# Optimization experiments

Measured on AMD Instinct MI355X. Metric: run time of the kernel, lower is better.

## Reference

```python
import jax, jax.numpy as jnp
import numpy as np
import math

NHEADS = 4


def _mab(Q, K, qw, qb, kw, kb, vw, vb, ow, ob, mask):
    """MAB2 from tripletformer: multi-head attention (head split via cat(split,0)),
    softmax scale uses sqrt(FULL dim_V), masked_fill(mask==0, -1e10), residual on
    the projected Q, then O + relu(fc_o(O))."""
    dv = qw.shape[1]
    dh = dv // NHEADS
    B, Nq, _ = Q.shape
    Nk = K.shape[1]
    Qh = (Q @ qw + qb).reshape(B, Nq, NHEADS, dh).transpose(0, 2, 1, 3)  # B,h,Nq,dh
    Kh = (K @ kw + kb).reshape(B, Nk, NHEADS, dh).transpose(0, 2, 1, 3)
    Vh = (K @ vw + vb).reshape(B, Nk, NHEADS, dh).transpose(0, 2, 1, 3)
    att = jnp.einsum('bhqd,bhkd->bhqk', Qh, Kh) * (1.0 / math.sqrt(dv))
    att = jnp.where(mask, att, jnp.asarray(-1e10, att.dtype))
    A = jax.nn.softmax(att, axis=-1)
    Oh = Qh + jnp.einsum('bhqk,bhkd->bhqd', A, Vh)
    O = Oh.transpose(0, 2, 1, 3).reshape(B, Nq, dv)
    return O + jax.nn.relu(O @ ow + ob)


def _forward(context_x, value, mask, obs_len, iff_w, iff_b, ind_points,
             q0w, q0b, k0w, k0b, v0w, v0b, o0w, o0b,
             q1w, q1b, k1w, k1b, v1w, v1b, o1w, o1b):
    B, L = context_x.shape
    D = value.shape[-1]
    mflat = mask.reshape(B, L * D)
    # stable stream compaction: observed entries first, original (time-major,
    # channel-minor) order preserved; truncate to static obs_len
    order = jnp.argsort(-mflat, axis=-1, stable=True)[:, :obs_len]  # (B, N)
    T = jnp.broadcast_to(context_x[:, :, None], (B, L, D)).reshape(B, L * D)
    C = jnp.broadcast_to(jnp.arange(D, dtype=jnp.int32), (B, L, D)).reshape(B, L * D)
    U = value.reshape(B, L * D)
    take = lambda a: jnp.take_along_axis(a, order, axis=-1)
    T_, U_, mk_ = take(T), take(U), take(mflat)
    Ch = jax.nn.one_hot(take(C), D, dtype=value.dtype)  # one_hot(num_classes=dim-2)
    X = jnp.concatenate([Ch, T_[..., None], U_[..., None]], axis=-1) * mk_[..., None]
    Y = jax.nn.relu(X @ iff_w + iff_b) * mk_[..., None]
    key_valid = mk_ > 0                        # (B, N)
    mask1 = key_valid[:, None, None, :]        # mab0: mask padded keys
    mask2 = key_valid[:, None, :, None]        # mab1: mask padded query rows
    Z = Y
    n_layers = ind_points.shape[0]
    for i in range(n_layers):
        I = jnp.broadcast_to(ind_points[i], (B,) + ind_points[i].shape)
        H = _mab(I, Z, q0w[i], q0b[i], k0w[i], k0b[i], v0w[i], v0b[i], o0w[i], o0b[i], mask1)
        Zn = _mab(Z, H, q1w[i], q1b[i], k1w[i], k1b[i], v1w[i], v1b[i], o1w[i], o1b[i], mask2)
        Z = Zn * mk_[..., None] + Z
    return Z, mk_[..., None]


def setup_inputs() -> dict:
    B, L, D, OBS, DK, M, NL = 16, 512, 41, 4096, 128, 128, 3
    key = jax.random.key(0)
    ks = jax.random.split(key, 16)
    context_x = jnp.sort(jax.random.uniform(ks[0], (B, L), dtype=jnp.float32), axis=-1)
    value = jax.random.normal(ks[1], (B, L, D), dtype=jnp.float32)
    # exactly OBS observed entries per batch row -> static packed length
    r = jax.random.uniform(ks[2], (B, L * D))
    kth = jnp.sort(r, axis=-1)[:, OBS]
    mask = (r < kth[:, None]).astype(jnp.float32).reshape(B, L, D)

    def w(k, shape, fan):
        return jax.random.normal(k, shape, dtype=jnp.float32) / math.sqrt(fan)

    inp = dict(
        context_x=context_x, value=value, mask=mask, obs_len=OBS,
        iff_w=w(ks[3], (D + 2, DK), D + 2), iff_b=jnp.zeros((DK,), jnp.float32),
        ind_points=w(ks[4], (NL, M, DK), DK),
    )
    for j, n in enumerate(['q0', 'k0', 'v0', 'o0', 'q1', 'k1', 'v1', 'o1']):
        inp[n + 'w'] = w(ks[5 + j], (NL, DK, DK), DK)
        inp[n + 'b'] = jnp.zeros((NL, DK), jnp.float32)
    return inp


def reference(context_x, value, mask, obs_len, iff_w, iff_b, ind_points,
              q0w, q0b, k0w, k0b, v0w, v0b, o0w, o0b,
              q1w, q1b, k1w, k1b, v1w, v1b, o1w, o1b):
    return _forward(context_x, value, mask, obs_len, iff_w, iff_b, ind_points,
                    q0w, q0b, k0w, k0b, v0w, v0b, o0w, o0b,
                    q1w, q1b, k1w, k1b, v1w, v1b, o1w, o1b)
```

## Files before the change

kernel.cpp:

```cpp
#include <hip/hip_runtime.h>
#include <math.h>

#define NBATCH 16
#define SEQL   512
#define DIM    41
#define LDFLAT (SEQL*DIM)
#define OBS    4096
#define DK     128
#define NH     4
#define DH     32

typedef short bf16x8 __attribute__((ext_vector_type(8)));
typedef short short8v __attribute__((ext_vector_type(8)));
typedef float floatx4 __attribute__((ext_vector_type(4)));

__device__ __forceinline__ short f2bf(float f) {
  union { float f; unsigned u; } v;
  v.f = f;
  unsigned r = (v.u + 0x7fffu + ((v.u >> 16) & 1u)) >> 16;
  return (short)r;
}
__device__ __forceinline__ float bf2f(short s) {
  union { unsigned u; float f; } v;
  v.u = ((unsigned)(unsigned short)s) << 16;
  return v.f;
}

__device__ __forceinline__ void stage_w(short* Wl, const short* __restrict__ Wt,
                                        int tid) {
#pragma unroll
  for (int i = tid * 8; i < 128 * 128; i += 2048)
    *(int4*)&Wl[(i >> 7) * 136 + (i & 127)] = *(const int4*)&Wt[i];
}
__device__ __forceinline__ void load_af(const short* Xl, int wv, int lm,
                                        int quad, bf16x8 af[4]) {
#pragma unroll
  for (int kc = 0; kc < 4; kc++)
    af[kc] = *(bf16x8*)&Xl[(wv * 16 + lm) * 136 + kc * 32 + quad * 8];
}
__device__ __forceinline__ void gemm8(const short* Wl, const bf16x8 af[4],
                                      int lm, int quad, floatx4 acc[8]) {
#pragma unroll
  for (int nt = 0; nt < 8; nt++) acc[nt] = (floatx4){0.f, 0.f, 0.f, 0.f};
#pragma unroll
  for (int kc = 0; kc < 4; kc++) {
    bf16x8 a = af[kc];
#pragma unroll
    for (int nt = 0; nt < 8; nt++) {
      bf16x8 b = *(bf16x8*)&Wl[(nt * 16 + lm) * 136 + kc * 32 + quad * 8];
      acc[nt] = __builtin_amdgcn_mfma_f32_16x16x32_bf16(a, b, acc[nt], 0, 0, 0);
    }
  }
}
__device__ __forceinline__ void store_sl(short* Sl, const floatx4 acc[8],
                                         const float* __restrict__ bias,
                                         int wv, int lm, int quad) {
#pragma unroll
  for (int nt = 0; nt < 8; nt++) {
    int col = nt * 16 + lm;
    float bn = bias[col];
#pragma unroll
    for (int r = 0; r < 4; r++)
      Sl[(wv * 16 + quad * 4 + r) * 136 + col] = f2bf(acc[nt][r] + bn);
  }
}
__device__ __forceinline__ void write_hs(const short* Sl,
                                         short* __restrict__ out, int rb,
                                         int nshift, int tid) {
  int rr = tid >> 2, hh = tid & 3;
  int r = rb + rr;
  int bb = r >> nshift, nn = r & ((1 << nshift) - 1);
  size_t o = (((size_t)(bb * NH + hh) << nshift) + nn) * 32;
#pragma unroll
  for (int j = 0; j < 4; j++)
    *(int4*)&out[o + j * 8] = *(int4*)&Sl[rr * 136 + hh * 32 + j * 8];
}

__global__ __launch_bounds__(256) void prep_weights_kernel(
    const float* __restrict__ q0w, const float* __restrict__ k0w,
    const float* __restrict__ v0w, const float* __restrict__ o0w,
    const float* __restrict__ q1w, const float* __restrict__ k1w,
    const float* __restrict__ v1w, const float* __restrict__ o1w,
    short* __restrict__ Wt) {
  __shared__ float Tl[128 * 132];
  int id = blockIdx.x, l = id >> 3, wi = id & 7;
  const float* s;
  switch (wi) {
    case 0: s = q0w; break; case 1: s = k0w; break;
    case 2: s = v0w; break; case 3: s = o0w; break;
    case 4: s = q1w; break; case 5: s = k1w; break;
    case 6: s = v1w; break; default: s = o1w; break;
  }
  s += (size_t)l * 16384;
  int tid = threadIdx.x;
  for (int i = tid * 4; i < 16384; i += 1024) {
    int k = i >> 7, n = i & 127;
    float4 x = *(const float4*)&s[i];
    Tl[k * 132 + n + 0] = x.x; Tl[k * 132 + n + 1] = x.y;
    Tl[k * 132 + n + 2] = x.z; Tl[k * 132 + n + 3] = x.w;
  }
  __syncthreads();
  short* dst = Wt + (size_t)id * 16384;
  int n = tid >> 1, k0 = (tid & 1) * 64;
  for (int jc = 0; jc < 8; jc++) {
    short8v t;
#pragma unroll
    for (int j = 0; j < 8; j++) t[j] = f2bf(Tl[(k0 + jc * 8 + j) * 132 + n]);
    *(short8v*)&dst[n * 128 + k0 + jc * 8] = t;
  }
}

__global__ __launch_bounds__(1024) void build_order_kernel(
    const float* __restrict__ mask, int* __restrict__ order,
    float* __restrict__ mk_out, float* __restrict__ mk_out2) {
  int b = blockIdx.x;
  const float* m = mask + (size_t)b * LDFLAT;
  int tid = threadIdx.x;
  int lane = tid & 63, w = tid >> 6;
  __shared__ int wsums[16];
  __shared__ int s_total_ones;
  __shared__ int s_chunk_ones;
  __shared__ int s_ones_base;
  __shared__ int s_zeros_base;

  int cnt = 0;
  for (int j = tid; j < LDFLAT; j += 1024) cnt += (m[j] > 0.f) ? 1 : 0;
  for (int off = 32; off > 0; off >>= 1) cnt += __shfl_xor(cnt, off);
  if (lane == 0) wsums[w] = cnt;
  __syncthreads();
  if (tid == 0) {
    int t = 0;
    for (int i = 0; i < 16; i++) t += wsums[i];
    s_total_ones = t; s_ones_base = 0; s_zeros_base = 0;
  }
  __syncthreads();
  int total_ones = s_total_ones;

  for (int c0 = 0; c0 < LDFLAT; c0 += 1024) {
    __syncthreads();
    int j = c0 + tid;
    bool valid = (j < LDFLAT);
    float mv = valid ? m[j] : 0.f;
    int one = (valid && mv > 0.f) ? 1 : 0;
    int v = one;
    for (int off = 1; off < 64; off <<= 1) {
      int t = __shfl_up(v, (unsigned)off);
      if (lane >= off) v += t;
    }
    if (lane == 63) wsums[w] = v;
    __syncthreads();
    if (tid == 0) {
      int run = 0;
      for (int i = 0; i < 16; i++) { int t = wsums[i]; wsums[i] = run; run += t; }
      s_chunk_ones = run;
    }
    __syncthreads();
    int ones_before = (v - one) + wsums[w];
    int ob = s_ones_base, zb = s_zeros_base, chunk_ones = s_chunk_ones;
    int rem = LDFLAT - c0;
    int chunk_valid = rem < 1024 ? rem : 1024;
    int valid_before = tid < rem ? tid : rem;
    if (valid) {
      int pos = one ? (ob + ones_before)
                    : (total_ones + zb + (valid_before - ones_before));
      if (pos < OBS) {
        order[b * OBS + pos] = j;
        mk_out[b * OBS + pos] = mv;
        mk_out2[b * OBS + pos] = mv;
      }
    }
    __syncthreads();
    if (tid == 0) {
      s_ones_base = ob + chunk_ones;
      s_zeros_base = zb + (chunk_valid - chunk_ones);
    }
  }
}

__global__ __launch_bounds__(256) void qh_proj_kernel(
    const float* __restrict__ indp, const short* __restrict__ Wt,
    const float* __restrict__ q0b, short* __restrict__ qh_b) {
  __shared__ __align__(16) short Xl[64 * 136];
  __shared__ __align__(16) short Wl[128 * 136];
  int l = blockIdx.y, rb = blockIdx.x * 64;
  const float* X = indp + (size_t)l * 16384 + (size_t)rb * 128;
  const short* W = Wt + (size_t)(l * 8) * 16384;
  const float* bias = q0b + (size_t)l * 128;
  short* out = qh_b + (size_t)l * 16384;
  int tid = threadIdx.x;
  for (int i = tid * 4; i < 64 * 128; i += 1024) {
    int rr = i >> 7, c = i & 127;
    float4 x = *(const float4*)&X[i];
    *(short4*)&Xl[rr * 136 + c] =
        make_short4(f2bf(x.x), f2bf(x.y), f2bf(x.z), f2bf(x.w));
  }
  stage_w(Wl, W, tid);
  __syncthreads();
  int wv = tid >> 6, lane = tid & 63, lm = lane & 15, quad = lane >> 4;
  bf16x8 af[4];
  load_af(Xl, wv, lm, quad, af);
  floatx4 acc[8];
  gemm8(Wl, af, lm, quad, acc);
  __syncthreads();
  store_sl(Wl, acc, bias, wv, lm, quad);
  __syncthreads();
  write_hs(Wl, out, rb, 7, tid);
}

__global__ __launch_bounds__(256) void fusedA_kernel(
    const int* __restrict__ order, const float* __restrict__ mk_g,
    const float* __restrict__ cx, const float* __restrict__ value,
    const float* __restrict__ iff_w, const float* __restrict__ iff_b,
    float* __restrict__ Z,
    const short* __restrict__ Wk, const float* __restrict__ kbias,
    short* __restrict__ Kb,
    const short* __restrict__ Wv, const float* __restrict__ vbias,
    short* __restrict__ Vb,
    const short* __restrict__ Wq, const float* __restrict__ qbias,
    short* __restrict__ Qb) {
  __shared__ __align__(16) short Xl[64 * 136];
  __shared__ __align__(16) short Wl[128 * 136];
  __shared__ int   rdd[64];
  __shared__ float rdt[64], rdu[64], rdm[64];
  int tid = threadIdx.x;
  int rb = blockIdx.x * 64;
  if (tid < 64) {
    int idx = rb + tid;
    int b = idx >> 12;
    int j = order[idx];
    int l = j / DIM;
    rdd[tid] = j - l * DIM;
    rdt[tid] = cx[b * SEQL + l];
    rdu[tid] = value[(size_t)b * LDFLAT + j];
    rdm[tid] = mk_g[idx];
  }
  stage_w(Wl, Wk, tid);
  __syncthreads();
  for (int i = tid; i < 64 * 128; i += 256) {
    int rr = i >> 7, k = i & 127;
    float y = iff_w[rdd[rr] * DK + k] + rdt[rr] * iff_w[41 * DK + k] +
              rdu[rr] * iff_w[42 * DK + k] + iff_b[k];
    float z = fmaxf(y, 0.f) * rdm[rr];
    Z[(size_t)(rb + rr) * DK + k] = z;
    Xl[rr * 136 + k] = f2bf(z);
  }
  __syncthreads();
  int wv = tid >> 6, lane = tid & 63, lm = lane & 15, quad = lane >> 4;
  bf16x8 af[4];
  load_af(Xl, wv, lm, quad, af);
  floatx4 acc[8];
  gemm8(Wl, af, lm, quad, acc);
  __syncthreads();
  store_sl(Wl, acc, kbias, wv, lm, quad);
  __syncthreads();
  write_hs(Wl, Kb, rb, 12, tid);
  __syncthreads();
  stage_w(Wl, Wv, tid);
  __syncthreads();
  gemm8(Wl, af, lm, quad, acc);
  __syncthreads();
  store_sl(Wl, acc, vbias, wv, lm, quad);
  __syncthreads();
  write_hs(Wl, Vb, rb, 12, tid);
  __syncthreads();
  stage_w(Wl, Wq, tid);
  __syncthreads();
  gemm8(Wl, af, lm, quad, acc);
  __syncthreads();
  store_sl(Wl, acc, qbias, wv, lm, quad);
  __syncthreads();
  write_hs(Wl, Qb, rb, 12, tid);
}

__global__ __launch_bounds__(256) void attn1_kernel(
    const short* __restrict__ Qh,
    const short* __restrict__ Kh, const short* __restrict__ Vh,
    const float* __restrict__ mk,
    float* __restrict__ Opart, float* __restrict__ mpart,
    float* __restrict__ lpart) {
  __shared__ __align__(16) short Ql[128 * 40];
  __shared__ __align__(16) short Kc[64 * 40];
  __shared__ __align__(16) short Vtc[32 * 72];
  __shared__ __align__(16) short Pl[128 * 72];
  __shared__ float mkc[64];
  int bh = blockIdx.x;
  int b = bh >> 2, h = bh & 3;
  int ks = blockIdx.y;
  int tid = threadIdx.x;
  int wv = tid >> 6, lane = tid & 63, lm = lane & 15, quad = lane >> 4;

  const short* qbg = Qh + (size_t)h * 128 * 32;
  for (int i = tid * 8; i < 128 * 32; i += 2048) {
    int r = i >> 5, c = i & 31;
    *(int4*)&Ql[r * 40 + c] = *(const int4*)&qbg[i];
  }
  __syncthreads();
  bf16x8 aq[2];
  aq[0] = *(bf16x8*)&Ql[(wv * 32 + lm) * 40 + quad * 8];
  aq[1] = *(bf16x8*)&Ql[(wv * 32 + 16 + lm) * 40 + quad * 8];

  float m_i[2][4], l_i[2][4];
  floatx4 oacc[2][2];
#pragma unroll
  for (int mt = 0; mt < 2; mt++) {
#pragma unroll
    for (int r = 0; r < 4; r++) { m_i[mt][r] = -1e30f; l_i[mt][r] = 0.f; }
    oacc[mt][0] = (floatx4){0.f, 0.f, 0.f, 0.f};
    oacc[mt][1] = (floatx4){0.f, 0.f, 0.f, 0.f};
  }
  const float scale = 0.08838834764831845f;
  const short* kbase = Kh + ((size_t)bh * OBS + ks * 512) * 32;
  const short* vbase = Vh + ((size_t)bh * OBS + ks * 512) * 32;
  const float* mkb = mk + (size_t)b * OBS + ks * 512;

  for (int ch = 0; ch < 8; ch++) {
    __syncthreads();
    {
      int i = tid * 8;
      int r = i >> 5, c = i & 31;
      *(int4*)&Kc[r * 40 + c] = *(const int4*)&kbase[ch * 2048 + i];
      int4 vv4 = *(const int4*)&vbase[ch * 2048 + i];
      short* vv = (short*)&vv4;
#pragma unroll
      for (int j = 0; j < 8; j++) Vtc[(c + j) * 72 + r] = vv[j];
    }
    if (tid < 64) mkc[tid] = mkb[ch * 64 + tid];
    __syncthreads();

    floatx4 sf[2][4];
#pragma unroll
    for (int nt = 0; nt < 4; nt++) {
      bf16x8 bfrag = *(bf16x8*)&Kc[(nt * 16 + lm) * 40 + quad * 8];
      floatx4 z = {0.f, 0.f, 0.f, 0.f};
      sf[0][nt] = __builtin_amdgcn_mfma_f32_16x16x32_bf16(aq[0], bfrag, z, 0, 0, 0);
      sf[1][nt] = __builtin_amdgcn_mfma_f32_16x16x32_bf16(aq[1], bfrag, z, 0, 0, 0);
    }
#pragma unroll
    for (int nt = 0; nt < 4; nt++) {
      float mkv = mkc[nt * 16 + lm];
      bool ok = mkv > 0.f;
#pragma unroll
      for (int mt = 0; mt < 2; mt++)
#pragma unroll
        for (int r = 0; r < 4; r++)
          sf[mt][nt][r] = ok ? sf[mt][nt][r] * scale : -1e10f;
    }
#pragma unroll
    for (int mt = 0; mt < 2; mt++) {
#pragma unroll
      for (int r = 0; r < 4; r++) {
        float mx = fmaxf(fmaxf(sf[mt][0][r], sf[mt][1][r]),
                         fmaxf(sf[mt][2][r], sf[mt][3][r]));
        mx = fmaxf(mx, __shfl_xor(mx, 1));
        mx = fmaxf(mx, __shfl_xor(mx, 2));
        mx = fmaxf(mx, __shfl_xor(mx, 4));
        mx = fmaxf(mx, __shfl_xor(mx, 8));
        float mn = fmaxf(m_i[mt][r], mx);
        float al = __expf(m_i[mt][r] - mn);
        float ps = 0.f;
#pragma unroll
        for (int nt = 0; nt < 4; nt++) {
          float p = __expf(sf[mt][nt][r] - mn);
          sf[mt][nt][r] = p;
          ps += p;
        }
        ps += __shfl_xor(ps, 1);
        ps += __shfl_xor(ps, 2);
        ps += __shfl_xor(ps, 4);
        ps += __shfl_xor(ps, 8);
        l_i[mt][r] = l_i[mt][r] * al + ps;
        m_i[mt][r] = mn;
        oacc[mt][0] *= al;
        oacc[mt][1] *= al;
      }
    }
#pragma unroll
    for (int mt = 0; mt < 2; mt++)
#pragma unroll
      for (int nt = 0; nt < 4; nt++)
#pragma unroll
        for (int r = 0; r < 4; r++)
          Pl[(wv * 32 + mt * 16 + quad * 4 + r) * 72 + nt * 16 + lm] =
              f2bf(sf[mt][nt][r]);
#pragma unroll
    for (int kc = 0; kc < 2; kc++) {
      bf16x8 vf0 = *(bf16x8*)&Vtc[lm * 72 + kc * 32 + quad * 8];
      bf16x8 vf1 = *(bf16x8*)&Vtc[(16 + lm) * 72 + kc * 32 + quad * 8];
#pragma unroll
      for (int mt = 0; mt < 2; mt++) {
        bf16x8 pf = *(bf16x8*)&Pl[(wv * 32 + mt * 16 + lm) * 72 + kc * 32 + quad * 8];
        oacc[mt][0] = __builtin_amdgcn_mfma_f32_16x16x32_bf16(pf, vf0, oacc[mt][0], 0, 0, 0);
        oacc[mt][1] = __builtin_amdgcn_mfma_f32_16x16x32_bf16(pf, vf1, oacc[mt][1], 0, 0, 0);
      }
    }
  }
  float* ob = Opart + (size_t)(ks * 64 + bh) * 128 * 32;
#pragma unroll
  for (int mt = 0; mt < 2; mt++) {
#pragma unroll
    for (int r = 0; r < 4; r++) {
      int row = wv * 32 + mt * 16 + quad * 4 + r;
      ob[(size_t)row * 32 + lm] = oacc[mt][0][r];
      ob[(size_t)row * 32 + 16 + lm] = oacc[mt][1][r];
      if (lm == 0) {
        mpart[(size_t)(ks * 64 + bh) * 128 + row] = m_i[mt][r];
        lpart[(size_t)(ks * 64 + bh) * 128 + row] = l_i[mt][r];
      }
    }
  }
}

__global__ __launch_bounds__(256) void fusedB_kernel(
    const float* __restrict__ Opart, const float* __restrict__ mpart,
    const float* __restrict__ lpart, const short* __restrict__ qh,
    const short* __restrict__ Wo, const float* __restrict__ obias,
    const short* __restrict__ Wk, const float* __restrict__ kbias,
    const short* __restrict__ Wv, const float* __restrict__ vbias,
    short* __restrict__ khb, short* __restrict__ vhb) {
  __shared__ __align__(16) short Xl[64 * 136];
  __shared__ __align__(16) short Wl[128 * 136];
  int tid = threadIdx.x;
  int rb = blockIdx.x * 64;
  int b = rb >> 7, n0 = rb & 127;
  {
    int rr = tid >> 2, hh = tid & 3;
    int n = n0 + rr;
    int bh = b * 4 + hh;
    float mv[8], lv[8], m = -1e30f;
#pragma unroll
    for (int s = 0; s < 8; s++) {
      mv[s] = mpart[(size_t)(s * 64 + bh) * 128 + n];
      lv[s] = lpart[(size_t)(s * 64 + bh) * 128 + n];
      m = fmaxf(m, mv[s]);
    }
    float l = 0.f;
    float oa[32];
#pragma unroll
    for (int d = 0; d < 32; d++) oa[d] = 0.f;
#pragma unroll
    for (int s = 0; s < 8; s++) {
      float w = __expf(mv[s] - m);
      l += lv[s] * w;
      const float* op = &Opart[((size_t)(s * 64 + bh) * 128 + n) * 32];
#pragma unroll
      for (int d4 = 0; d4 < 8; d4++) {
        float4 v = *(const float4*)&op[d4 * 4];
        oa[d4 * 4 + 0] += v.x * w; oa[d4 * 4 + 1] += v.y * w;
        oa[d4 * 4 + 2] += v.z * w; oa[d4 * 4 + 3] += v.w * w;
      }
    }
    float li = 1.f / l;
    const short* qp = &qh[((size_t)hh * 128 + n) * 32];
#pragma unroll
    for (int d = 0; d < 32; d++)
      Xl[rr * 136 + hh * 32 + d] = f2bf(bf2f(qp[d]) + oa[d] * li);
  }
  stage_w(Wl, Wo, tid);
  __syncthreads();
  int wv = tid >> 6, lane = tid & 63, lm = lane & 15, quad = lane >> 4;
  bf16x8 af[4];
  load_af(Xl, wv, lm, quad, af);
  floatx4 acc[8];
  gemm8(Wl, af, lm, quad, acc);
  __syncthreads();
#pragma unroll
  for (int nt = 0; nt < 8; nt++) {
    int col = nt * 16 + lm;
    float bn = obias[col];
#pragma unroll
    for (int r = 0; r < 4; r++) {
      int row = wv * 16 + quad * 4 + r;
      float ov = bf2f(Xl[row * 136 + col]);
      Wl[row * 136 + col] = f2bf(ov + fmaxf(acc[nt][r] + bn, 0.f));
    }
  }
  __syncthreads();
  for (int i = tid * 8; i < 64 * 128; i += 2048)
    *(int4*)&Xl[(i >> 7) * 136 + (i & 127)] = *(int4*)&Wl[(i >> 7) * 136 + (i & 127)];
  __syncthreads();
  load_af(Xl, wv, lm, quad, af);
  stage_w(Wl, Wk, tid);
  __syncthreads();
  gemm8(Wl, af, lm, quad, acc);
  __syncthreads();
  store_sl(Wl, acc, kbias, wv, lm, quad);
  __syncthreads();
  write_hs(Wl, khb, rb, 7, tid);
  __syncthreads();
  stage_w(Wl, Wv, tid);
  __syncthreads();
  gemm8(Wl, af, lm, quad, acc);
  __syncthreads();
  store_sl(Wl, acc, vbias, wv, lm, quad);
  __syncthreads();
  write_hs(Wl, vhb, rb, 7, tid);
}

__global__ __launch_bounds__(256) void attn2_kernel(
    const short* __restrict__ Qh, const short* __restrict__ Kh,
    const short* __restrict__ Vh, short* __restrict__ O) {
  __shared__ __align__(16) short Kl[128 * 40];
  __shared__ __align__(16) short Vt[32 * 136];
  __shared__ __align__(16) short Ql[64 * 40];
  __shared__ __align__(16) short Pl[64 * 136];
  int bh = blockIdx.x;
  int b = bh >> 2, h = bh & 3;
  int q0 = blockIdx.y * 64;
  int tid = threadIdx.x;
  int wv = tid >> 6, lane = tid & 63, lm = lane & 15, quad = lane >> 4;
  const short* kb = Kh + (size_t)bh * 128 * 32;
  const short* vb = Vh + (size_t)bh * 128 * 32;
  const short* qb = Qh + ((size_t)bh * OBS + q0) * 32;

  for (int i = tid * 8; i < 128 * 32; i += 2048) {
    int r = i >> 5, c = i & 31;
    *(int4*)&Kl[r * 40 + c] = *(const int4*)&kb[i];
  }
  for (int i = tid * 8; i < 64 * 32; i += 2048) {
    int r = i >> 5, c = i & 31;
    *(int4*)&Ql[r * 40 + c] = *(const int4*)&qb[i];
  }
  for (int i = tid * 8; i < 128 * 32; i += 2048) {
    int r = i >> 5, c = i & 31;
    int4 vv4 = *(const int4*)&vb[i];
    short* vv = (short*)&vv4;
#pragma unroll
    for (int j = 0; j < 8; j++) Vt[(c + j) * 136 + r] = vv[j];
  }
  __syncthreads();

  const float scale = 0.08838834764831845f;
  bf16x8 afrag = *(bf16x8*)&Ql[(wv * 16 + lm) * 40 + quad * 8];
  floatx4 sf[8];
#pragma unroll
  for (int nt = 0; nt < 8; nt++) {
    bf16x8 bfrag = *(bf16x8*)&Kl[(nt * 16 + lm) * 40 + quad * 8];
    floatx4 z = {0.f, 0.f, 0.f, 0.f};
    sf[nt] = __builtin_amdgcn_mfma_f32_16x16x32_bf16(afrag, bfrag, z, 0, 0, 0);
  }
#pragma unroll
  for (int nt = 0; nt < 8; nt++) sf[nt] *= scale;
  float linv[4];
#pragma unroll
  for (int r = 0; r < 4; r++) {
    float mx = sf[0][r];
#pragma unroll
    for (int nt = 1; nt < 8; nt++) mx = fmaxf(mx, sf[nt][r]);
    mx = fmaxf(mx, __shfl_xor(mx, 1));
    mx = fmaxf(mx, __shfl_xor(mx, 2));
    mx = fmaxf(mx, __shfl_xor(mx, 4));
    mx = fmaxf(mx, __shfl_xor(mx, 8));
    float sum = 0.f;
#pragma unroll
    for (int nt = 0; nt < 8; nt++) {
      float p = __expf(sf[nt][r] - mx);
      sf[nt][r] = p;
      sum += p;
    }
    sum += __shfl_xor(sum, 1);
    sum += __shfl_xor(sum, 2);
    sum += __shfl_xor(sum, 4);
    sum += __shfl_xor(sum, 8);
    linv[r] = 1.f / sum;
  }
#pragma unroll
  for (int nt = 0; nt < 8; nt++)
#pragma unroll
    for (int r = 0; r < 4; r++)
      Pl[(wv * 16 + quad * 4 + r) * 136 + nt * 16 + lm] = f2bf(sf[nt][r]);
  __syncthreads();

  floatx4 oacc[2] = {{0.f, 0.f, 0.f, 0.f}, {0.f, 0.f, 0.f, 0.f}};
#pragma unroll
  for (int kc = 0; kc < 4; kc++) {
    bf16x8 pf = *(bf16x8*)&Pl[(wv * 16 + lm) * 136 + kc * 32 + quad * 8];
#pragma unroll
    for (int nt2 = 0; nt2 < 2; nt2++) {
      bf16x8 vf = *(bf16x8*)&Vt[(nt2 * 16 + lm) * 136 + kc * 32 + quad * 8];
      oacc[nt2] = __builtin_amdgcn_mfma_f32_16x16x32_bf16(pf, vf, oacc[nt2], 0, 0, 0);
    }
  }
  __syncthreads();
  short* Ol = Pl;
#pragma unroll
  for (int nt2 = 0; nt2 < 2; nt2++) {
#pragma unroll
    for (int r = 0; r < 4; r++) {
      int qrow = wv * 16 + quad * 4 + r;
      float q = bf2f(Ql[qrow * 40 + nt2 * 16 + lm]);
      Ol[qrow * 136 + nt2 * 16 + lm] = f2bf(q + oacc[nt2][r] * linv[r]);
    }
  }
  __syncthreads();
  int rr = tid >> 2, seg = tid & 3;
  size_t o = ((size_t)b * OBS + q0 + rr) * 128 + h * 32 + seg * 8;
  *(int4*)&O[o] = *(int4*)&Ol[rr * 136 + seg * 8];
}

__global__ __launch_bounds__(256) void fusedC_kernel(
    const short* __restrict__ Ob, const short* __restrict__ Wo,
    const float* __restrict__ obias, const float* __restrict__ mk,
    const float* __restrict__ Zin, float* __restrict__ Zout,
    const short* __restrict__ Wk, const float* __restrict__ kbias,
    short* __restrict__ Kb,
    const short* __restrict__ Wv, const float* __restrict__ vbias,
    short* __restrict__ Vb,
    const short* __restrict__ Wq, const float* __restrict__ qbias,
    short* __restrict__ Qb) {
  __shared__ __align__(16) short Xl[64 * 136];
  __shared__ __align__(16) short Wl[128 * 136];
  int tid = threadIdx.x;
  int rb = blockIdx.x * 64;
  for (int i = tid * 8; i < 64 * 128; i += 2048) {
    int rr = i >> 7, c = i & 127;
    *(int4*)&Xl[rr * 136 + c] = *(const int4*)&Ob[(size_t)(rb + rr) * 128 + c];
  }
  stage_w(Wl, Wo, tid);
  __syncthreads();
  int wv = tid >> 6, lane = tid & 63, lm = lane & 15, quad = lane >> 4;
  bf16x8 af[4];
  load_af(Xl, wv, lm, quad, af);
  floatx4 acc[8];
  gemm8(Wl, af, lm, quad, acc);
  __syncthreads();
  float* Fl = (float*)Wl;
#pragma unroll
  for (int nt = 0; nt < 8; nt++) {
    int col = nt * 16 + lm;
    float bn = obias[col];
#pragma unroll
    for (int r = 0; r < 4; r++) {
      int row = wv * 16 + quad * 4 + r;
      int gr = rb + row;
      float ov = bf2f(Xl[row * 136 + col]);
      float f = ov + fmaxf(acc[nt][r] + bn, 0.f);
      Fl[row * 132 + col] = Zin[(size_t)gr * 128 + col] + f * mk[gr];
    }
  }
  __syncthreads();
  {
    int rr = tid >> 2, seg = tid & 3;
    int gr = rb + rr;
#pragma unroll
    for (int j = 0; j < 8; j++) {
      float4 f = *(float4*)&Fl[rr * 132 + seg * 32 + j * 4];
      *(float4*)&Zout[(size_t)gr * 128 + seg * 32 + j * 4] = f;
      *(short4*)&Xl[rr * 136 + seg * 32 + j * 4] =
          make_short4(f2bf(f.x), f2bf(f.y), f2bf(f.z), f2bf(f.w));
    }
  }
  if (Wk == nullptr) return;
  __syncthreads();
  load_af(Xl, wv, lm, quad, af);
  stage_w(Wl, Wk, tid);
  __syncthreads();
  gemm8(Wl, af, lm, quad, acc);
  __syncthreads();
  store_sl(Wl, acc, kbias, wv, lm, quad);
  __syncthreads();
  write_hs(Wl, Kb, rb, 12, tid);
  __syncthreads();
  stage_w(Wl, Wv, tid);
  __syncthreads();
  gemm8(Wl, af, lm, quad, acc);
  __syncthreads();
  store_sl(Wl, acc, vbias, wv, lm, quad);
  __syncthreads();
  write_hs(Wl, Vb, rb, 12, tid);
  __syncthreads();
  stage_w(Wl, Wq, tid);
  __syncthreads();
  gemm8(Wl, af, lm, quad, acc);
  __syncthreads();
  store_sl(Wl, acc, qbias, wv, lm, quad);
  __syncthreads();
  write_hs(Wl, Qb, rb, 12, tid);
}

extern "C" void kernel_launch(void* const* d_in, const int* in_sizes, int n_in,
                              void* d_out, int out_size, void* d_ws,
                              size_t ws_size, hipStream_t stream) {
  const float* cx    = (const float*)d_in[0];
  const float* value = (const float*)d_in[1];
  const float* mask  = (const float*)d_in[2];
  const float* iff_w = (const float*)d_in[4];
  const float* iff_b = (const float*)d_in[5];
  const float* indp  = (const float*)d_in[6];
  const float* q0w = (const float*)d_in[7];  const float* q0b = (const float*)d_in[8];
  const float* k0w = (const float*)d_in[9];  const float* k0b = (const float*)d_in[10];
  const float* v0w = (const float*)d_in[11]; const float* v0b = (const float*)d_in[12];
  const float* o0w = (const float*)d_in[13]; const float* o0b = (const float*)d_in[14];
  const float* q1w = (const float*)d_in[15]; const float* q1b = (const float*)d_in[16];
  const float* k1w = (const float*)d_in[17]; const float* k1b = (const float*)d_in[18];
  const float* v1w = (const float*)d_in[19]; const float* v1b = (const float*)d_in[20];
  const float* o1w = (const float*)d_in[21]; const float* o1b = (const float*)d_in[22];

  char* ws = (char*)d_ws;
  short* Wt    = (short*)ws;  ws += (size_t)24 * 16384 * 2;
  int*   order = (int*)ws;    ws += (size_t)NBATCH * OBS * 4;
  float* mk_g  = (float*)ws;  ws += (size_t)NBATCH * OBS * 4;
  float* Z     = (float*)ws;  ws += (size_t)NBATCH * OBS * DK * 4;
  short* Qb    = (short*)ws;  ws += (size_t)NBATCH * OBS * DK * 2;
  short* Kb    = (short*)ws;  ws += (size_t)NBATCH * OBS * DK * 2;
  short* Vb    = (short*)ws;  ws += (size_t)NBATCH * OBS * DK * 2;
  short* Ob    = (short*)ws;  ws += (size_t)NBATCH * OBS * DK * 2;
  short* qh_b  = (short*)ws;  ws += (size_t)3 * 128 * DK * 2;
  short* khb   = (short*)ws;  ws += (size_t)NBATCH * NH * 128 * DH * 2;
  short* vhb   = (short*)ws;  ws += (size_t)NBATCH * NH * 128 * DH * 2;
  float* Opart = (float*)ws;  ws += (size_t)8 * 64 * 128 * 32 * 4;
  float* mpart = (float*)ws;  ws += (size_t)8 * 64 * 128 * 4;
  float* lpart = (float*)ws;  ws += (size_t)8 * 64 * 128 * 4;

  float* outZ  = (float*)d_out;
  float* outMk = outZ + (size_t)NBATCH * OBS * DK;

  prep_weights_kernel<<<24, 256, 0, stream>>>(q0w, k0w, v0w, o0w, q1w, k1w,
                                              v1w, o1w, Wt);
  build_order_kernel<<<NBATCH, 1024, 0, stream>>>(mask, order, mk_g, outMk);
  qh_proj_kernel<<<dim3(2, 3), 256, 0, stream>>>(indp, Wt, q0b, qh_b);

  const short* W[3][8];
  for (int l = 0; l < 3; l++)
    for (int wi = 0; wi < 8; wi++) W[l][wi] = Wt + (size_t)(l * 8 + wi) * 16384;

  fusedA_kernel<<<1024, 256, 0, stream>>>(
      order, mk_g, cx, value, iff_w, iff_b, Z,
      W[0][1], k0b, Kb, W[0][2], v0b, Vb, W[0][4], q1b, Qb);

  for (int l = 0; l < 3; l++) {
    attn1_kernel<<<dim3(64, 8), 256, 0, stream>>>(
        qh_b + (size_t)l * 16384, Kb, Vb, mk_g, Opart, mpart, lpart);
    fusedB_kernel<<<32, 256, 0, stream>>>(
        Opart, mpart, lpart, qh_b + (size_t)l * 16384,
        W[l][3], o0b + (size_t)l * 128,
        W[l][5], k1b + (size_t)l * 128,
        W[l][6], v1b + (size_t)l * 128, khb, vhb);
    attn2_kernel<<<dim3(64, 64), 256, 0, stream>>>(Qb, khb, vhb, Ob);
    if (l < 2) {
      fusedC_kernel<<<1024, 256, 0, stream>>>(
          Ob, W[l][7], o1b + (size_t)l * 128, mk_g, Z, Z,
          W[l + 1][1], k0b + (size_t)(l + 1) * 128, Kb,
          W[l + 1][2], v0b + (size_t)(l + 1) * 128, Vb,
          W[l + 1][4], q1b + (size_t)(l + 1) * 128, Qb);
    } else {
      fusedC_kernel<<<1024, 256, 0, stream>>>(
          Ob, W[l][7], o1b + (size_t)l * 128, mk_g, Z, outZ,
          nullptr, nullptr, nullptr, nullptr, nullptr, nullptr,
          nullptr, nullptr, nullptr);
    }
  }
}
```

Measured before the change: 530.8 us.

## Prefetch next weight tile into registers and store GEMM outputs directly to global

Weight matrices for the next projection (V, Q, K) are loaded into registers while the current MFMA GEMM runs, then committed to shared memory, which overlaps global loads with compute. The LDS staging round-trip for outputs is removed: results are written straight to head-split global layout from the accumulators. fusedC reads its input A-fragments and residuals directly from global memory. The cost is more register pressure and narrower (2-byte, scattered) global stores in place of coalesced 16-byte writes.

New measurement: 572.2 us. +7.8%, slower.

```diff
diff --git a/kernel.cpp b/kernel.cpp
--- a/kernel.cpp
+++ b/kernel.cpp
@@ -32,11 +32,33 @@
   for (int i = tid * 8; i < 128 * 128; i += 2048)
     *(int4*)&Wl[(i >> 7) * 136 + (i & 127)] = *(const int4*)&Wt[i];
 }
+__device__ __forceinline__ void prefetch_w(const short* __restrict__ Wt,
+                                           int tid, int4 wreg[8]) {
+#pragma unroll
+  for (int j = 0; j < 8; j++)
+    wreg[j] = *(const int4*)&Wt[tid * 8 + j * 2048];
+}
+__device__ __forceinline__ void commit_w(short* Wl, int tid,
+                                         const int4 wreg[8]) {
+#pragma unroll
+  for (int j = 0; j < 8; j++) {
+    int i = tid * 8 + j * 2048;
+    *(int4*)&Wl[(i >> 7) * 136 + (i & 127)] = wreg[j];
+  }
+}
 __device__ __forceinline__ void load_af(const short* Xl, int wv, int lm,
                                         int quad, bf16x8 af[4]) {
 #pragma unroll
   for (int kc = 0; kc < 4; kc++)
     af[kc] = *(bf16x8*)&Xl[(wv * 16 + lm) * 136 + kc * 32 + quad * 8];
+}
+__device__ __forceinline__ void load_af_global(const short* __restrict__ X,
+                                               int row0, int wv, int lm,
+                                               int quad, bf16x8 af[4]) {
+  const short* rp = X + (size_t)(row0 + wv * 16 + lm) * 128;
+#pragma unroll
+  for (int kc = 0; kc < 4; kc++)
+    af[kc] = *(const bf16x8*)&rp[kc * 32 + quad * 8];
 }
 __device__ __forceinline__ void gemm8(const short* Wl, const bf16x8 af[4],
                                       int lm, int quad, floatx4 acc[8]) {
@@ -52,28 +74,25 @@
     }
   }
 }
-__device__ __forceinline__ void store_sl(short* Sl, const floatx4 acc[8],
+__device__ __forceinline__ void store_hs(short* __restrict__ out,
+                                         const floatx4 acc[8],
                                          const float* __restrict__ bias,
-                                         int wv, int lm, int quad) {
+                                         int rb, int nshift, int wv, int lm,
+                                         int quad) {
 #pragma unroll
   for (int nt = 0; nt < 8; nt++) {
     int col = nt * 16 + lm;
     float bn = bias[col];
-#pragma unroll
-    for (int r = 0; r < 4; r++)
-      Sl[(wv * 16 + quad * 4 + r) * 136 + col] = f2bf(acc[nt][r] + bn);
-  }
-}
-__device__ __forceinline__ void write_hs(const short* Sl,
-                                         short* __restrict__ out, int rb,
-                                         int nshift, int tid) {
-  int rr = tid >> 2, hh = tid & 3;
-  int r = rb + rr;
-  int bb = r >> nshift, nn = r & ((1 << nshift) - 1);
-  size_t o = (((size_t)(bb * NH + hh) << nshift) + nn) * 32;
-#pragma unroll
-  for (int j = 0; j < 4; j++)
-    *(int4*)&out[o + j * 8] = *(int4*)&Sl[rr * 136 + hh * 32 + j * 8];
+    int hh = nt >> 1;
+    int dd = (nt & 1) * 16 + lm;
+#pragma unroll
+    for (int r = 0; r < 4; r++) {
+      int gr = rb + wv * 16 + quad * 4 + r;
+      int bb = gr >> nshift, nn = gr & ((1 << nshift) - 1);
+      out[(((size_t)(bb * NH + hh) << nshift) + nn) * 32 + dd] =
+          f2bf(acc[nt][r] + bn);
+    }
+  }
 }
 
 __global__ __launch_bounds__(256) void prep_weights_kernel(
@@ -201,10 +220,7 @@
   load_af(Xl, wv, lm, quad, af);
   floatx4 acc[8];
   gemm8(Wl, af, lm, quad, acc);
-  __syncthreads();
-  store_sl(Wl, acc, bias, wv, lm, quad);
-  __syncthreads();
-  write_hs(Wl, out, rb, 7, tid);
+  store_hs(out, acc, bias, rb, 7, wv, lm, quad);
 }
 
 __global__ __launch_bounds__(256) void fusedA_kernel(
@@ -248,28 +264,22 @@
   int wv = tid >> 6, lane = tid & 63, lm = lane & 15, quad = lane >> 4;
   bf16x8 af[4];
   load_af(Xl, wv, lm, quad, af);
+  int4 wreg[8];
+  prefetch_w(Wv, tid, wreg);
   floatx4 acc[8];
   gemm8(Wl, af, lm, quad, acc);
-  __syncthreads();
-  store_sl(Wl, acc, kbias, wv, lm, quad);
-  __syncthreads();
-  write_hs(Wl, Kb, rb, 12, tid);
-  __syncthreads();
-  stage_w(Wl, Wv, tid);
-  __syncthreads();
-  gemm8(Wl, af, lm, quad, acc);
-  __syncthreads();
-  store_sl(Wl, acc, vbias, wv, lm, quad);
-  __syncthreads();
-  write_hs(Wl, Vb, rb, 12, tid);
-  __syncthreads();
-  stage_w(Wl, Wq, tid);
-  __syncthreads();
-  gemm8(Wl, af, lm, quad, acc);
-  __syncthreads();
-  store_sl(Wl, acc, qbias, wv, lm, quad);
-  __syncthreads();
-  write_hs(Wl, Qb, rb, 12, tid);
+  store_hs(Kb, acc, kbias, rb, 12, wv, lm, quad);
+  __syncthreads();
+  commit_w(Wl, tid, wreg);
+  prefetch_w(Wq, tid, wreg);
+  __syncthreads();
+  gemm8(Wl, af, lm, quad, acc);
+  store_hs(Vb, acc, vbias, rb, 12, wv, lm, quad);
+  __syncthreads();
+  commit_w(Wl, tid, wreg);
+  __syncthreads();
+  gemm8(Wl, af, lm, quad, acc);
+  store_hs(Qb, acc, qbias, rb, 12, wv, lm, quad);
 }
 
 __global__ __launch_bounds__(256) void attn1_kernel(
@@ -456,13 +466,14 @@
       Xl[rr * 136 + hh * 32 + d] = f2bf(bf2f(qp[d]) + oa[d] * li);
   }
   stage_w(Wl, Wo, tid);
+  int4 wreg[8];
+  prefetch_w(Wk, tid, wreg);
   __syncthreads();
   int wv = tid >> 6, lane = tid & 63, lm = lane & 15, quad = lane >> 4;
   bf16x8 af[4];
   load_af(Xl, wv, lm, quad, af);
   floatx4 acc[8];
   gemm8(Wl, af, lm, quad, acc);
-  __syncthreads();
 #pragma unroll
   for (int nt = 0; nt < 8; nt++) {
     int col = nt * 16 + lm;
@@ -471,29 +482,21 @@
     for (int r = 0; r < 4; r++) {
       int row = wv * 16 + quad * 4 + r;
       float ov = bf2f(Xl[row * 136 + col]);
-      Wl[row * 136 + col] = f2bf(ov + fmaxf(acc[nt][r] + bn, 0.f));
-    }
-  }
-  __syncthreads();
-  for (int i = tid * 8; i < 64 * 128; i += 2048)
-    *(int4*)&Xl[(i >> 7) * 136 + (i & 127)] = *(int4*)&Wl[(i >> 7) * 136 + (i & 127)];
-  __syncthreads();
+      Xl[row * 136 + col] = f2bf(ov + fmaxf(acc[nt][r] + bn, 0.f));
+    }
+  }
+  __syncthreads();
+  commit_w(Wl, tid, wreg);
+  prefetch_w(Wv, tid, wreg);
   load_af(Xl, wv, lm, quad, af);
-  stage_w(Wl, Wk, tid);
-  __syncthreads();
-  gemm8(Wl, af, lm, quad, acc);
-  __syncthreads();
-  store_sl(Wl, acc, kbias, wv, lm, quad);
-  __syncthreads();
-  write_hs(Wl, khb, rb, 7, tid);
-  __syncthreads();
-  stage_w(Wl, Wv, tid);
-  __syncthreads();
-  gemm8(Wl, af, lm, quad, acc);
-  __syncthreads();
-  store_sl(Wl, acc, vbias, wv, lm, quad);
-  __syncthreads();
-  write_hs(Wl, vhb, rb, 7, tid);
+  __syncthreads();
+  gemm8(Wl, af, lm, quad, acc);
+  store_hs(khb, acc, kbias, rb, 7, wv, lm, quad);
+  __syncthreads();
+  commit_w(Wl, tid, wreg);
+  __syncthreads();
+  gemm8(Wl, af, lm, quad, acc);
+  store_hs(vhb, acc, vbias, rb, 7, wv, lm, quad);
 }
 
 __global__ __launch_bounds__(256) void attn2_kernel(
@@ -580,21 +583,16 @@
       oacc[nt2] = __builtin_amdgcn_mfma_f32_16x16x32_bf16(pf, vf, oacc[nt2], 0, 0, 0);
     }
   }
-  __syncthreads();
-  short* Ol = Pl;
 #pragma unroll
   for (int nt2 = 0; nt2 < 2; nt2++) {
 #pragma unroll
     for (int r = 0; r < 4; r++) {
       int qrow = wv * 16 + quad * 4 + r;
       float q = bf2f(Ql[qrow * 40 + nt2 * 16 + lm]);
-      Ol[qrow * 136 + nt2 * 16 + lm] = f2bf(q + oacc[nt2][r] * linv[r]);
-    }
-  }
-  __syncthreads();
-  int rr = tid >> 2, seg = tid & 3;
-  size_t o = ((size_t)b * OBS + q0 + rr) * 128 + h * 32 + seg * 8;
-  *(int4*)&O[o] = *(int4*)&Ol[rr * 136 + seg * 8];
+      O[((size_t)b * OBS + q0 + qrow) * 128 + h * 32 + nt2 * 16 + lm] =
+          f2bf(q + oacc[nt2][r] * linv[r]);
+    }
+  }
 }
 
 __global__ __launch_bounds__(256) void fusedC_kernel(
@@ -611,19 +609,18 @@
   __shared__ __align__(16) short Wl[128 * 136];
   int tid = threadIdx.x;
   int rb = blockIdx.x * 64;
-  for (int i = tid * 8; i < 64 * 128; i += 2048) {
-    int rr = i >> 7, c = i & 127;
-    *(int4*)&Xl[rr * 136 + c] = *(const int4*)&Ob[(size_t)(rb + rr) * 128 + c];
-  }
+  int wv = tid >> 6, lane = tid & 63, lm = lane & 15, quad = lane >> 4;
   stage_w(Wl, Wo, tid);
-  __syncthreads();
-  int wv = tid >> 6, lane = tid & 63, lm = lane & 15, quad = lane >> 4;
   bf16x8 af[4];
-  load_af(Xl, wv, lm, quad, af);
+  load_af_global(Ob, rb, wv, lm, quad, af);
+  int4 wreg[8];
+  if (Wk) prefetch_w(Wk, tid, wreg);
+  __syncthreads();
   floatx4 acc[8];
   gemm8(Wl, af, lm, quad, acc);
-  __syncthreads();
-  float* Fl = (float*)Wl;
+  float mkv[4];
+#pragma unroll
+  for (int r = 0; r < 4; r++) mkv[r] = mk[rb + wv * 16 + quad * 4 + r];
 #pragma unroll
   for (int nt = 0; nt < 8; nt++) {
     int col = nt * 16 + lm;
@@ -631,50 +628,33 @@
 #pragma unroll
     for (int r = 0; r < 4; r++) {
       int row = wv * 16 + quad * 4 + r;
-      int gr = rb + row;
-      float ov = bf2f(Xl[row * 136 + col]);
+      size_t gi = (size_t)(rb + row) * 128 + col;
+      float ov = bf2f(Ob[gi]);
       float f = ov + fmaxf(acc[nt][r] + bn, 0.f);
-      Fl[row * 132 + col] = Zin[(size_t)gr * 128 + col] + f * mk[gr];
-    }
-  }
-  __syncthreads();
-  {
-    int rr = tid >> 2, seg = tid & 3;
-    int gr = rb + rr;
-#pragma unroll
-    for (int j = 0; j < 8; j++) {
-      float4 f = *(float4*)&Fl[rr * 132 + seg * 32 + j * 4];
-      *(float4*)&Zout[(size_t)gr * 128 + seg * 32 + j * 4] = f;
-      *(short4*)&Xl[rr * 136 + seg * 32 + j * 4] =
-          make_short4(f2bf(f.x), f2bf(f.y), f2bf(f.z), f2bf(f.w));
+      float zn = Zin[gi] + f * mkv[r];
+      Zout[gi] = zn;
+      if (Wk) Xl[row * 136 + col] = f2bf(zn);
     }
   }
   if (Wk == nullptr) return;
   __syncthreads();
+  commit_w(Wl, tid, wreg);
+  prefetch_w(Wv, tid, wreg);
   load_af(Xl, wv, lm, quad, af);
-  stage_w(Wl, Wk, tid);
-  __syncthreads();
-  gemm8(Wl, af, lm, quad, acc);
-  __syncthreads();
-  store_sl(Wl, acc, kbias, wv, lm, quad);
-  __syncthreads();
-  write_hs(Wl, Kb, rb, 12, tid);
-  __syncthreads();
-  stage_w(Wl, Wv, tid);
-  __syncthreads();
-  gemm8(Wl, af, lm, quad, acc);
-  __syncthreads();
-  store_sl(Wl, acc, vbias, wv, lm, quad);
-  __syncthreads();
-  write_hs(Wl, Vb, rb, 12, tid);
-  __syncthreads();
-  stage_w(Wl, Wq, tid);
-  __syncthreads();
-  gemm8(Wl, af, lm, quad, acc);
-  __syncthreads();
-  store_sl(Wl, acc, qbias, wv, lm, quad);
-  __syncthreads();
-  write_hs(Wl, Qb, rb, 12, tid);
+  __syncthreads();
+  gemm8(Wl, af, lm, quad, acc);
+  store_hs(Kb, acc, kbias, rb, 12, wv, lm, quad);
+  __syncthreads();
+  commit_w(Wl, tid, wreg);
+  prefetch_w(Wq, tid, wreg);
+  __syncthreads();
+  gemm8(Wl, af, lm, quad, acc);
+  store_hs(Vb, acc, vbias, rb, 12, wv, lm, quad);
+  __syncthreads();
+  commit_w(Wl, tid, wreg);
+  __syncthreads();
+  gemm8(Wl, af, lm, quad, acc);
+  store_hs(Qb, acc, qbias, rb, 12, wv, lm, quad);
 }
 
 extern "C" void kernel_launch(void* const* d_in, const int* in_sizes, int n_in,
```

## Prefetch next projection weights into registers and drop wave-local barriers

Applied to the files above, without the earlier changes.

Adds register-staged prefetch of the next 128x128 weight matrix (Wv, Wq, Wk) while the current MFMA GEMM runs, then commits it to LDS after a barrier. This overlaps global weight loads with compute instead of serialising them. It also removes __syncthreads calls where each wave only reads LDS rows it wrote itself, drops an LDS-to-LDS copy in the layer-transition kernel, and moves the residual Zin read into a vectorised loop. The risk is extra register pressure from holding eight int4 per thread, and a race if any removed barrier actually guarded data shared across waves.

Result: slower. 629.0 us (+18.5%).

```diff
diff --git a/kernel.cpp b/kernel.cpp
--- a/kernel.cpp
+++ b/kernel.cpp
@@ -31,6 +31,20 @@
 #pragma unroll
   for (int i = tid * 8; i < 128 * 128; i += 2048)
     *(int4*)&Wl[(i >> 7) * 136 + (i & 127)] = *(const int4*)&Wt[i];
+}
+__device__ __forceinline__ void prefetch_w(const short* __restrict__ Wt,
+                                           int tid, int4 wreg[8]) {
+#pragma unroll
+  for (int j = 0; j < 8; j++)
+    wreg[j] = *(const int4*)&Wt[tid * 8 + j * 2048];
+}
+__device__ __forceinline__ void commit_w(short* Wl, int tid,
+                                         const int4 wreg[8]) {
+#pragma unroll
+  for (int j = 0; j < 8; j++) {
+    int i = tid * 8 + j * 2048;
+    *(int4*)&Wl[(i >> 7) * 136 + (i & 127)] = wreg[j];
+  }
 }
 __device__ __forceinline__ void load_af(const short* Xl, int wv, int lm,
                                         int quad, bf16x8 af[4]) {
@@ -203,7 +217,6 @@
   gemm8(Wl, af, lm, quad, acc);
   __syncthreads();
   store_sl(Wl, acc, bias, wv, lm, quad);
-  __syncthreads();
   write_hs(Wl, out, rb, 7, tid);
 }
 
@@ -248,27 +261,27 @@
   int wv = tid >> 6, lane = tid & 63, lm = lane & 15, quad = lane >> 4;
   bf16x8 af[4];
   load_af(Xl, wv, lm, quad, af);
+  int4 wreg[8];
+  prefetch_w(Wv, tid, wreg);
   floatx4 acc[8];
   gemm8(Wl, af, lm, quad, acc);
   __syncthreads();
   store_sl(Wl, acc, kbias, wv, lm, quad);
-  __syncthreads();
   write_hs(Wl, Kb, rb, 12, tid);
   __syncthreads();
-  stage_w(Wl, Wv, tid);
+  commit_w(Wl, tid, wreg);
+  prefetch_w(Wq, tid, wreg);
   __syncthreads();
   gemm8(Wl, af, lm, quad, acc);
   __syncthreads();
   store_sl(Wl, acc, vbias, wv, lm, quad);
-  __syncthreads();
   write_hs(Wl, Vb, rb, 12, tid);
   __syncthreads();
-  stage_w(Wl, Wq, tid);
+  commit_w(Wl, tid, wreg);
   __syncthreads();
   gemm8(Wl, af, lm, quad, acc);
   __syncthreads();
   store_sl(Wl, acc, qbias, wv, lm, quad);
-  __syncthreads();
   write_hs(Wl, Qb, rb, 12, tid);
 }
 
@@ -456,13 +469,14 @@
       Xl[rr * 136 + hh * 32 + d] = f2bf(bf2f(qp[d]) + oa[d] * li);
   }
   stage_w(Wl, Wo, tid);
+  int4 wreg[8];
+  prefetch_w(Wk, tid, wreg);
   __syncthreads();
   int wv = tid >> 6, lane = tid & 63, lm = lane & 15, quad = lane >> 4;
   bf16x8 af[4];
   load_af(Xl, wv, lm, quad, af);
   floatx4 acc[8];
   gemm8(Wl, af, lm, quad, acc);
-  __syncthreads();
 #pragma unroll
   for (int nt = 0; nt < 8; nt++) {
     int col = nt * 16 + lm;
@@ -471,28 +485,24 @@
     for (int r = 0; r < 4; r++) {
       int row = wv * 16 + quad * 4 + r;
       float ov = bf2f(Xl[row * 136 + col]);
-      Wl[row * 136 + col] = f2bf(ov + fmaxf(acc[nt][r] + bn, 0.f));
-    }
-  }
-  __syncthreads();
-  for (int i = tid * 8; i < 64 * 128; i += 2048)
-    *(int4*)&Xl[(i >> 7) * 136 + (i & 127)] = *(int4*)&Wl[(i >> 7) * 136 + (i & 127)];
-  __syncthreads();
+      Xl[row * 136 + col] = f2bf(ov + fmaxf(acc[nt][r] + bn, 0.f));
+    }
+  }
   load_af(Xl, wv, lm, quad, af);
-  stage_w(Wl, Wk, tid);
+  __syncthreads();
+  commit_w(Wl, tid, wreg);
+  prefetch_w(Wv, tid, wreg);
   __syncthreads();
   gemm8(Wl, af, lm, quad, acc);
   __syncthreads();
   store_sl(Wl, acc, kbias, wv, lm, quad);
-  __syncthreads();
   write_hs(Wl, khb, rb, 7, tid);
   __syncthreads();
-  stage_w(Wl, Wv, tid);
+  commit_w(Wl, tid, wreg);
   __syncthreads();
   gemm8(Wl, af, lm, quad, acc);
   __syncthreads();
   store_sl(Wl, acc, vbias, wv, lm, quad);
-  __syncthreads();
   write_hs(Wl, vhb, rb, 7, tid);
 }
 
@@ -568,7 +578,6 @@
 #pragma unroll
     for (int r = 0; r < 4; r++)
       Pl[(wv * 16 + quad * 4 + r) * 136 + nt * 16 + lm] = f2bf(sf[nt][r]);
-  __syncthreads();
 
   floatx4 oacc[2] = {{0.f, 0.f, 0.f, 0.f}, {0.f, 0.f, 0.f, 0.f}};
 #pragma unroll
@@ -580,7 +589,6 @@
       oacc[nt2] = __builtin_amdgcn_mfma_f32_16x16x32_bf16(pf, vf, oacc[nt2], 0, 0, 0);
     }
   }
-  __syncthreads();
   short* Ol = Pl;
 #pragma unroll
   for (int nt2 = 0; nt2 < 2; nt2++) {
@@ -591,7 +599,6 @@
       Ol[qrow * 136 + nt2 * 16 + lm] = f2bf(q + oacc[nt2][r] * linv[r]);
     }
   }
-  __syncthreads();
   int rr = tid >> 2, seg = tid & 3;
   size_t o = ((size_t)b * OBS + q0 + rr) * 128 + h * 32 + seg * 8;
   *(int4*)&O[o] = *(int4*)&Ol[rr * 136 + seg * 8];
@@ -611,13 +618,15 @@
   __shared__ __align__(16) short Wl[128 * 136];
   int tid = threadIdx.x;
   int rb = blockIdx.x * 64;
+  int wv = tid >> 6, lane = tid & 63, lm = lane & 15, quad = lane >> 4;
   for (int i = tid * 8; i < 64 * 128; i += 2048) {
     int rr = i >> 7, c = i & 127;
     *(int4*)&Xl[rr * 136 + c] = *(const int4*)&Ob[(size_t)(rb + rr) * 128 + c];
   }
   stage_w(Wl, Wo, tid);
-  __syncthreads();
-  int wv = tid >> 6, lane = tid & 63, lm = lane & 15, quad = lane >> 4;
+  int4 wreg[8];
+  if (Wk) prefetch_w(Wk, tid, wreg);
+  __syncthreads();
   bf16x8 af[4];
   load_af(Xl, wv, lm, quad, af);
   floatx4 acc[8];
@@ -631,49 +640,49 @@
 #pragma unroll
     for (int r = 0; r < 4; r++) {
       int row = wv * 16 + quad * 4 + r;
-      int gr = rb + row;
       float ov = bf2f(Xl[row * 136 + col]);
-      float f = ov + fmaxf(acc[nt][r] + bn, 0.f);
-      Fl[row * 132 + col] = Zin[(size_t)gr * 128 + col] + f * mk[gr];
-    }
-  }
-  __syncthreads();
+      Fl[row * 132 + col] = ov + fmaxf(acc[nt][r] + bn, 0.f);
+    }
+  }
   {
     int rr = tid >> 2, seg = tid & 3;
     int gr = rb + rr;
+    float mkv = mk[gr];
 #pragma unroll
     for (int j = 0; j < 8; j++) {
       float4 f = *(float4*)&Fl[rr * 132 + seg * 32 + j * 4];
-      *(float4*)&Zout[(size_t)gr * 128 + seg * 32 + j * 4] = f;
-      *(short4*)&Xl[rr * 136 + seg * 32 + j * 4] =
-          make_short4(f2bf(f.x), f2bf(f.y), f2bf(f.z), f2bf(f.w));
+      float4 z = *(const float4*)&Zin[(size_t)gr * 128 + seg * 32 + j * 4];
+      z.x += f.x * mkv; z.y += f.y * mkv; z.z += f.z * mkv; z.w += f.w * mkv;
+      *(float4*)&Zout[(size_t)gr * 128 + seg * 32 + j * 4] = z;
+      if (Wk)
+        *(short4*)&Xl[rr * 136 + seg * 32 + j * 4] =
+            make_short4(f2bf(z.x), f2bf(z.y), f2bf(z.z), f2bf(z.w));
     }
   }
   if (Wk == nullptr) return;
-  __syncthreads();
   load_af(Xl, wv, lm, quad, af);
-  stage_w(Wl, Wk, tid);
+  __syncthreads();
+  commit_w(Wl, tid, wreg);
+  prefetch_w(Wv, tid, wreg);
   __syncthreads();
   gemm8(Wl, af, lm, quad, acc);
   __syncthreads();
   store_sl(Wl, acc, kbias, wv, lm, quad);
-  __syncthreads();
   write_hs(Wl, Kb, rb, 12, tid);
   __syncthreads();
-  stage_w(Wl, Wv, tid);
+  commit_w(Wl, tid, wreg);
+  prefetch_w(Wq, tid, wreg);
   __syncthreads();
   gemm8(Wl, af, lm, quad, acc);
   __syncthreads();
   store_sl(Wl, acc, vbias, wv, lm, quad);
-  __syncthreads();
   write_hs(Wl, Vb, rb, 12, tid);
   __syncthreads();
-  stage_w(Wl, Wq, tid);
+  commit_w(Wl, tid, wreg);
   __syncthreads();
   gemm8(Wl, af, lm, quad, acc);
   __syncthreads();
   store_sl(Wl, acc, qbias, wv, lm, quad);
-  __syncthreads();
   write_hs(Wl, Qb, rb, 12, tid);
 }
 
```
